# Performance work log

Hardware: AMD Instinct MI355X
Metric: run time of the kernel (lower is better)

## Reference

```python
import jax, jax.numpy as jnp
import numpy as np

B, L, D, H = 2, 4096, 768, 12
Dh = D // H


def setup_inputs() -> dict:
    key = jax.random.key(0)
    k1, k2, k3 = jax.random.split(key, 3)
    x = jax.random.normal(k1, (B, L, D), dtype=jnp.float32)
    Wqkv = jax.random.normal(k2, (D, 3 * D), dtype=jnp.float32) * 0.02
    bqkv = jnp.zeros((3 * D,), dtype=jnp.float32)
    Wo = jax.random.normal(k3, (D, D), dtype=jnp.float32) * 0.02
    bo = jnp.zeros((D,), dtype=jnp.float32)
    return {"x": x, "Wqkv": Wqkv, "bqkv": bqkv, "Wo": Wo, "bo": bo}


def reference(x, Wqkv, bqkv, Wo, bo):
    Bs, Ls, Ds = x.shape
    # fused QKV projection
    qkv = x @ Wqkv + bqkv  # [B, L, 3D]
    q, k, v = jnp.split(qkv, 3, axis=2)
    q = q.reshape(Bs, Ls, H, Dh)
    k = k.reshape(Bs, Ls, H, Dh)
    v = v.reshape(Bs, Ls, H, Dh)
    # scaled dot-product attention with causal mask (fp32 softmax, as flax dpa with dtype=float32)
    scale = 1.0 / np.sqrt(Dh)
    scores = jnp.einsum('bqhd,bkhd->bhqk', q, k) * scale  # [B, H, L, L]
    causal = jnp.tril(jnp.ones((Ls, Ls), dtype=bool))
    big_neg = jnp.finfo(jnp.float32).min
    scores = jnp.where(causal[None, None, :, :], scores, big_neg)
    attn = jax.nn.softmax(scores, axis=-1)
    y = jnp.einsum('bhqk,bkhd->bqhd', attn, v)  # [B, L, H, Dh]
    y = y.reshape(Bs, Ls, Ds)
    # output projection
    return y @ Wo + bo
```

## Files before the change

### kernel.cpp

```cpp
#include <hip/hip_runtime.h>
#include <hip/hip_bf16.h>
#include <stdint.h>

#define BB 2
#define LL 4096
#define DD 768
#define HH 12
#define DH 64
#define MM (BB * LL)
#define NQKV (3 * DD)
#define KK 768
#define PLANE ((size_t)BB * HH * LL * DH)
#define SQSCALE 0.1803368801111204f

typedef __attribute__((ext_vector_type(8))) short bf16x8;
typedef __attribute__((ext_vector_type(4))) float f32x4;

__device__ __forceinline__ float bf2f(uint16_t u) {
  union { uint32_t u; float f; } c; c.u = ((uint32_t)u) << 16; return c.f;
}
__device__ __forceinline__ uint16_t f2bf(float f) {
  union { float f; uint32_t u; } c; c.f = f;
  return (uint16_t)((c.u + 0x7FFFu + ((c.u >> 16) & 1u)) >> 16);
}
__device__ __forceinline__ uint32_t cvt2(float a, float b) {
  __hip_bfloat162 h = __float22bfloat162_rn(make_float2(a, b));
  union { __hip_bfloat162 h; uint32_t u; } c; c.h = h; return c.u;
}

union H8 { uint16_t h[8]; uint32_t w[4]; uint4 v; };
union B8 { uint2 d[2]; bf16x8 v; };

template <bool F32>
__device__ __forceinline__ H8 load8(const void* p, size_t idx) {
  H8 r;
  if (F32) {
    const float* f = (const float*)p + idx;
    float4 a = *(const float4*)f;
    float4 b = *(const float4*)(f + 4);
    r.w[0] = cvt2(a.x, a.y); r.w[1] = cvt2(a.z, a.w);
    r.w[2] = cvt2(b.x, b.y); r.w[3] = cvt2(b.z, b.w);
  } else {
    r.v = *(const uint4*)((const uint16_t*)p + idx);
  }
  return r;
}

__device__ __forceinline__ void g2l16(const uint16_t* g, uint16_t* l) {
  __builtin_amdgcn_global_load_lds((const __attribute__((address_space(1))) void*)g,
                                   (__attribute__((address_space(3))) void*)l,
                                   16, 0, 0);
}

__global__ void detect_k(const uint16_t* __restrict__ x, int* __restrict__ flag) {
  __shared__ int cnt;
  if (threadIdx.x == 0) cnt = 0;
  __syncthreads();
  int c = 0;
  for (int i = threadIdx.x; i < 4096; i += 256) {
    int e = (x[i] >> 7) & 0xFF;
    if (e == 0xFF || e > 133 || e < 100) c++;
  }
  atomicAdd(&cnt, c);
  __syncthreads();
  if (threadIdx.x == 0) *flag = (cnt > 512) ? 1 : 0;
}

__global__ __launch_bounds__(256) void prep_k(const void* __restrict__ x,
                                              uint16_t* __restrict__ xbf,
                                              const void* __restrict__ Wqkv,
                                              uint16_t* __restrict__ wqkvT,
                                              const void* __restrict__ Wo,
                                              uint16_t* __restrict__ woT,
                                              const int* __restrict__ flag) {
  __shared__ uint16_t Ts[64][65];
  const int fl = *flag;
  const int id = blockIdx.x;
  const int tid = threadIdx.x;
  if (id < 768) {
    size_t base = (size_t)id * 1024 + tid;
#pragma unroll
    for (int j = 0; j < 4; ++j) {
      size_t i = base + j * 256;
      H8 v = fl ? load8<true>(x, i * 8) : load8<false>(x, i * 8);
      *(uint4*)(xbf + i * 8) = v.v;
    }
    return;
  }
  const void* W;
  uint16_t* WT;
  int N, widx;
  if (id < 1200) { W = Wqkv; WT = wqkvT; N = NQKV; widx = id - 768; }
  else           { W = Wo;   WT = woT;   N = DD;   widx = id - 1200; }
  const int nb = N / 64;
  const int n0 = (widx % nb) * 64, k0 = (widx / nb) * 64;
#pragma unroll
  for (int j = 0; j < 16; ++j) {
    int idx = tid + j * 256;
    int r = idx >> 6, c = idx & 63;
    size_t gi = (size_t)(k0 + r) * N + n0 + c;
    float v = fl ? ((const float*)W)[gi] : bf2f(((const uint16_t*)W)[gi]);
    Ts[c][r] = f2bf(v);
  }
  __syncthreads();
#pragma unroll
  for (int j = 0; j < 16; ++j) {
    int idx = tid + j * 256;
    int n = idx >> 6, k = idx & 63;
    WT[(size_t)(n0 + n) * KK + k0 + k] = Ts[n][k];
  }
}

__device__ __forceinline__ void gemm128_core(const uint16_t* __restrict__ A,
                                             const uint16_t* __restrict__ BT,
                                             int m0, int n0,
                                             uint16_t* As, uint16_t* Bs,
                                             f32x4 acc[4][4]) {
  const int tid = threadIdx.x, lane = tid & 63, w = tid >> 6;
  const int quad = lane >> 4, c16 = lane & 15;
  const int wm = w >> 1, wn = w & 1;
  const int srow = lane >> 2, schunk = lane & 3;
  const int rsw = (c16 >> 1) & 3;
  for (int k0 = 0; k0 < KK; k0 += 32) {
#pragma unroll
    for (int i = 0; i < 2; ++i) {
      int row = w * 32 + i * 16 + srow;
      int gch = schunk ^ ((row >> 1) & 3);
      g2l16(A + (size_t)(m0 + row) * KK + k0 + gch * 8, As + (w * 32 + i * 16) * 32);
      g2l16(BT + (size_t)(n0 + row) * KK + k0 + gch * 8, Bs + (w * 32 + i * 16) * 32);
    }
    __syncthreads();
    bf16x8 a[4], b[4];
#pragma unroll
    for (int i = 0; i < 4; ++i) {
      a[i] = *(const bf16x8*)(As + (wm * 64 + i * 16 + c16) * 32 + ((quad ^ rsw) * 8));
      b[i] = *(const bf16x8*)(Bs + (wn * 64 + i * 16 + c16) * 32 + ((quad ^ rsw) * 8));
    }
#pragma unroll
    for (int i = 0; i < 4; ++i)
#pragma unroll
      for (int f = 0; f < 4; ++f)
        acc[i][f] = __builtin_amdgcn_mfma_f32_16x16x32_bf16(a[i], b[f], acc[i][f], 0, 0, 0);
    __syncthreads();
  }
}

__global__ __launch_bounds__(256) void qkv128_k(const uint16_t* __restrict__ X,
                                                const uint16_t* __restrict__ WT,
                                                const void* __restrict__ bias,
                                                uint16_t* __restrict__ planes,
                                                const int* __restrict__ flag) {
  __shared__ __align__(16) uint16_t As[128 * 32];
  __shared__ __align__(16) uint16_t Bs[128 * 32];
  __shared__ __align__(16) uint16_t Ts[64][136];
  const int fl = *flag;
  const int m0 = blockIdx.x * 128, n0 = blockIdx.y * 128;
  f32x4 acc[4][4];
#pragma unroll
  for (int i = 0; i < 4; ++i)
#pragma unroll
    for (int f = 0; f < 4; ++f) acc[i][f] = (f32x4){0.f, 0.f, 0.f, 0.f};
  gemm128_core(X, WT, m0, n0, As, Bs, acc);

  const int tid = threadIdx.x, lane = tid & 63, w = tid >> 6;
  const int quad = lane >> 4, c16 = lane & 15;
  const int wm = w >> 1, wn = w & 1;
  const int which = (n0 >= 2 * DD) ? 2 : (n0 >= DD ? 1 : 0);

  if (which < 2) {
    uint16_t* dst = planes + (size_t)which * PLANE;
    const float sc = (which == 0) ? SQSCALE : 1.0f;
#pragma unroll
    for (int f = 0; f < 4; ++f) {
      int n = n0 + wn * 64 + f * 16 + c16;
      float bv = fl ? ((const float*)bias)[n] : bf2f(((const uint16_t*)bias)[n]);
      int rem = n - which * DD;
      int hh = rem >> 6, dd = rem & 63;
#pragma unroll
      for (int i = 0; i < 4; ++i) {
        uint32_t pa = cvt2((acc[i][f][0] + bv) * sc, (acc[i][f][1] + bv) * sc);
        uint32_t pb = cvt2((acc[i][f][2] + bv) * sc, (acc[i][f][3] + bv) * sc);
        int m = m0 + wm * 64 + i * 16 + quad * 4;
        int b = m >> 12, l = m & (LL - 1);
        uint16_t* base = dst + ((size_t)(b * HH + hh) * LL + l) * DH + dd;
        base[0 * DH] = (uint16_t)pa;
        base[1 * DH] = (uint16_t)(pa >> 16);
        base[2 * DH] = (uint16_t)pb;
        base[3 * DH] = (uint16_t)(pb >> 16);
      }
    }
  } else {
    uint16_t* vtp = planes + 2 * PLANE;
    const int l0 = m0 & (LL - 1), bb = m0 >> 12;
    for (int half = 0; half < 2; ++half) {
      __syncthreads();
      if (wn == half) {
#pragma unroll
        for (int f = 0; f < 4; ++f) {
          int n = n0 + half * 64 + f * 16 + c16;
          float bv = fl ? ((const float*)bias)[n] : bf2f(((const uint16_t*)bias)[n]);
#pragma unroll
          for (int i = 0; i < 4; ++i) {
            uint32_t pa = cvt2(acc[i][f][0] + bv, acc[i][f][1] + bv);
            uint32_t pb = cvt2(acc[i][f][2] + bv, acc[i][f][3] + bv);
            *(uint2*)(&Ts[f * 16 + c16][wm * 64 + i * 16 + quad * 4]) = make_uint2(pa, pb);
          }
        }
      }
      __syncthreads();
#pragma unroll
      for (int j = 0; j < 4; ++j) {
        int idx = tid + j * 256;
        int nl = idx >> 4, ch = idx & 15;
        int rem = n0 + half * 64 + nl - 2 * DD;
        int hh = rem >> 6, dd = rem & 63;
        uint4 val = *(const uint4*)(&Ts[nl][ch * 8]);
        *(uint4*)(vtp + ((size_t)(bb * HH + hh) * DH + dd) * LL + l0 + ch * 8) = val;
      }
    }
  }
}

__global__ __launch_bounds__(256) void attn_k(const uint16_t* __restrict__ planes,
                                              uint16_t* __restrict__ y) {
  __shared__ __align__(16) uint16_t Ks[2][64 * 64];
  __shared__ __align__(16) uint16_t Vt[2][64 * 64];
  __shared__ __align__(16) uint16_t Ps[4][16 * 64];
  const int p = blockIdx.x;
  const int bh = blockIdx.y;
  const uint16_t* qb = planes + (size_t)bh * LL * DH;
  const uint16_t* kb = qb + PLANE;
  const uint16_t* vtb = planes + 2 * PLANE + (size_t)bh * DH * LL;
  const int tid = threadIdx.x, lane = tid & 63, wv = tid >> 6;
  const int quad = lane >> 4, c16 = lane & 15;
  const int r0 = tid >> 3, c0 = tid & 7;
  const int sw0 = r0 & 7;
  const int swf = c16 & 7;
  uint16_t* Psb = Ps[wv];
  const int b = bh / HH, hh = bh - b * HH;
  const int pwbase = c16 * 64;
  const int prd0 = pwbase + (((2 * quad) ^ c16) << 2);
  const int prd1 = pwbase + (((2 * quad + 1) ^ c16) << 2);
  const int prd2 = pwbase + (((8 + 2 * quad) ^ c16) << 2);
  const int prd3 = pwbase + (((8 + 2 * quad + 1) ^ c16) << 2);

  for (int pass = 0; pass < 2; ++pass) {
    const int qi = pass ? p : 63 - p;
    const int q0 = qi * 64;
    const size_t qoff = (size_t)(q0 + wv * 16 + c16) * DH;
    bf16x8 qf0 = *(const bf16x8*)(qb + qoff + quad * 8);
    bf16x8 qf1 = *(const bf16x8*)(qb + qoff + 32 + quad * 8);

    f32x4 o[4];
#pragma unroll
    for (int g = 0; g < 4; ++g) o[g] = (f32x4){0.f, 0.f, 0.f, 0.f};
    float l_i = 0.f;

    uint4 kr0 = *(const uint4*)(kb + (size_t)r0 * DH + c0 * 8);
    uint4 kr1 = *(const uint4*)(kb + (size_t)(r0 + 32) * DH + c0 * 8);
    uint4 vr0 = *(const uint4*)(vtb + (size_t)r0 * LL + c0 * 8);
    uint4 vr1 = *(const uint4*)(vtb + (size_t)(r0 + 32) * LL + c0 * 8);

    for (int t = 0; t <= qi; ++t) {
      uint16_t* kd = Ks[t & 1];
      uint16_t* vd = Vt[t & 1];
      *(uint4*)(kd + r0 * 64 + (c0 ^ sw0) * 8) = kr0;
      *(uint4*)(kd + (r0 + 32) * 64 + (c0 ^ sw0) * 8) = kr1;
      *(uint4*)(vd + r0 * 64 + (c0 ^ sw0) * 8) = vr0;
      *(uint4*)(vd + (r0 + 32) * 64 + (c0 ^ sw0) * 8) = vr1;
      if (t < qi) {
        int t64 = (t + 1) * 64;
        kr0 = *(const uint4*)(kb + (size_t)(t64 + r0) * DH + c0 * 8);
        kr1 = *(const uint4*)(kb + (size_t)(t64 + r0 + 32) * DH + c0 * 8);
        vr0 = *(const uint4*)(vtb + (size_t)r0 * LL + t64 + c0 * 8);
        vr1 = *(const uint4*)(vtb + (size_t)(r0 + 32) * LL + t64 + c0 * 8);
      }
      __syncthreads();

      f32x4 s[4];
#pragma unroll
      for (int f = 0; f < 4; ++f) {
        const uint16_t* krow = kd + (f * 16 + c16) * 64;
        bf16x8 k0f = *(const bf16x8*)(krow + ((quad ^ swf) * 8));
        bf16x8 k1f = *(const bf16x8*)(krow + (((quad + 4) ^ swf) * 8));
        f32x4 z = {0.f, 0.f, 0.f, 0.f};
        z = __builtin_amdgcn_mfma_f32_16x16x32_bf16(k0f, qf0, z, 0, 0, 0);
        z = __builtin_amdgcn_mfma_f32_16x16x32_bf16(k1f, qf1, z, 0, 0, 0);
        s[f] = z;
      }
      const int qg = q0 + wv * 16 + c16;
      if (t == qi) {
#pragma unroll
        for (int f = 0; f < 4; ++f) {
          int key0 = t * 64 + f * 16 + quad * 4;
#pragma unroll
          for (int r = 0; r < 4; ++r) {
            float pv = exp2f(s[f][r]);
            pv = (key0 + r <= qg) ? pv : 0.f;
            s[f][r] = pv;
            l_i += pv;
          }
        }
      } else {
#pragma unroll
        for (int f = 0; f < 4; ++f)
#pragma unroll
          for (int r = 0; r < 4; ++r) {
            float pv = exp2f(s[f][r]);
            s[f][r] = pv;
            l_i += pv;
          }
      }
#pragma unroll
      for (int f = 0; f < 4; ++f) {
        uint32_t w0 = cvt2(s[f][0], s[f][1]);
        uint32_t w1 = cvt2(s[f][2], s[f][3]);
        *(uint2*)(Psb + pwbase + (((f * 4 + quad) ^ c16) << 2)) = make_uint2(w0, w1);
      }
      __asm__ __volatile__("s_waitcnt lgkmcnt(0)" ::: "memory");
      B8 p0, p1;
      p0.d[0] = *(const uint2*)(Psb + prd0);
      p0.d[1] = *(const uint2*)(Psb + prd1);
      p1.d[0] = *(const uint2*)(Psb + prd2);
      p1.d[1] = *(const uint2*)(Psb + prd3);
#pragma unroll
      for (int g = 0; g < 4; ++g) {
        const uint16_t* vrow = vd + (g * 16 + c16) * 64;
        bf16x8 v0 = *(const bf16x8*)(vrow + ((quad ^ swf) * 8));
        bf16x8 v1 = *(const bf16x8*)(vrow + (((quad + 4) ^ swf) * 8));
        o[g] = __builtin_amdgcn_mfma_f32_16x16x32_bf16(p0.v, v0, o[g], 0, 0, 0);
        o[g] = __builtin_amdgcn_mfma_f32_16x16x32_bf16(p1.v, v1, o[g], 0, 0, 0);
      }
    }

    l_i += __shfl_xor(l_i, 16);
    l_i += __shfl_xor(l_i, 32);
    float inv[4];
#pragma unroll
    for (int r = 0; r < 4; ++r)
      inv[r] = 1.f / __shfl(l_i, (quad << 4) + quad * 4 + r);
#pragma unroll
    for (int g = 0; g < 4; ++g) {
      uint32_t pa = cvt2(o[g][0] * inv[0], o[g][1] * inv[1]);
      uint32_t pb = cvt2(o[g][2] * inv[2], o[g][3] * inv[3]);
      int l = q0 + wv * 16 + quad * 4;
      uint16_t* base = y + ((size_t)(b * LL + l)) * DD + hh * DH + g * 16 + c16;
      base[0 * DD] = (uint16_t)pa;
      base[1 * DD] = (uint16_t)(pa >> 16);
      base[2 * DD] = (uint16_t)pb;
      base[3 * DD] = (uint16_t)(pb >> 16);
    }
    __syncthreads();
  }
}

__global__ __launch_bounds__(256) void out128_k(const uint16_t* __restrict__ Y,
                                                const uint16_t* __restrict__ WT,
                                                const void* __restrict__ bias,
                                                void* __restrict__ out,
                                                const int* __restrict__ flag) {
  __shared__ __align__(16) uint16_t As[128 * 32];
  __shared__ __align__(16) uint16_t Bs[128 * 32];
  const int fl = *flag;
  const int m0 = blockIdx.x * 128, n0 = blockIdx.y * 128;
  f32x4 acc[4][4];
#pragma unroll
  for (int i = 0; i < 4; ++i)
#pragma unroll
    for (int f = 0; f < 4; ++f) acc[i][f] = (f32x4){0.f, 0.f, 0.f, 0.f};
  gemm128_core(Y, WT, m0, n0, As, Bs, acc);
  const int lane = threadIdx.x & 63, w = threadIdx.x >> 6;
  const int quad = lane >> 4, c16 = lane & 15;
  const int wm = w >> 1, wn = w & 1;
#pragma unroll
  for (int f = 0; f < 4; ++f) {
    int n = n0 + wn * 64 + f * 16 + c16;
    float bv = fl ? ((const float*)bias)[n] : bf2f(((const uint16_t*)bias)[n]);
#pragma unroll
    for (int i = 0; i < 4; ++i) {
      int m = m0 + wm * 64 + i * 16 + quad * 4;
      if (fl) {
        float* base = (float*)out + (size_t)m * DD + n;
#pragma unroll
        for (int r = 0; r < 4; ++r) base[r * DD] = acc[i][f][r] + bv;
      } else {
        uint32_t pa = cvt2(acc[i][f][0] + bv, acc[i][f][1] + bv);
        uint32_t pb = cvt2(acc[i][f][2] + bv, acc[i][f][3] + bv);
        uint16_t* base = (uint16_t*)out + (size_t)m * DD + n;
        base[0 * DD] = (uint16_t)pa;
        base[1 * DD] = (uint16_t)(pa >> 16);
        base[2 * DD] = (uint16_t)pb;
        base[3 * DD] = (uint16_t)(pb >> 16);
      }
    }
  }
}

extern "C" void kernel_launch(void* const* d_in, const int* in_sizes, int n_in,
                              void* d_out, int out_size, void* d_ws, size_t ws_size,
                              hipStream_t stream) {
  const void* x    = d_in[0];
  const void* Wqkv = d_in[1];
  const void* bqkv = d_in[2];
  const void* Wo   = d_in[3];
  const void* bo   = d_in[4];
  int* flagp = (int*)d_ws;
  uint16_t* planes = (uint16_t*)((char*)d_ws + 64);
  uint16_t* y_ws   = planes + 3 * PLANE;
  uint16_t* wqkvT  = y_ws + (size_t)MM * DD;
  uint16_t* woT    = wqkvT + (size_t)NQKV * KK;
  uint16_t* xbf    = y_ws;

  detect_k<<<1, 256, 0, stream>>>((const uint16_t*)x, flagp);
  prep_k<<<1344, 256, 0, stream>>>(x, xbf, Wqkv, wqkvT, Wo, woT, flagp);
  qkv128_k<<<dim3(MM / 128, NQKV / 128), 256, 0, stream>>>(xbf, wqkvT, bqkv, planes, flagp);
  attn_k<<<dim3(32, BB * HH), 256, 0, stream>>>(planes, y_ws);
  out128_k<<<dim3(MM / 128, DD / 128), 256, 0, stream>>>(y_ws, woT, bo, d_out, flagp);
}
```

Measured before the change: 271.0 us.

## Use fragment-major LDS layout with direct global-to-LDS loads in GEMMs and attention

Reorganizes shared-memory tiles into MFMA-fragment-major blocks of 512 elements, so each lane reads its 16-byte fragment contiguously without XOR swizzling. The GEMM core now steps K by 64 per barrier pair, halving the number of synchronizations. Attention K/V tiles are double-buffered through direct global-to-LDS copies instead of register staging plus LDS stores. The output projection switches to 128x64 tiles for more blocks. The copies are issued as narrow fragment rows, which may reduce global coalescing, and the qkv kernel reuses the same shared memory for the V transpose.

```diff
diff --git a/kernel.cpp b/kernel.cpp
--- a/kernel.cpp
+++ b/kernel.cpp
@@ -114,33 +114,47 @@
 __device__ __forceinline__ void gemm128_core(const uint16_t* __restrict__ A,
                                              const uint16_t* __restrict__ BT,
                                              int m0, int n0,
-                                             uint16_t* As, uint16_t* Bs,
+                                             uint16_t* Af, uint16_t* Bf,
                                              f32x4 acc[4][4]) {
   const int tid = threadIdx.x, lane = tid & 63, w = tid >> 6;
-  const int quad = lane >> 4, c16 = lane & 15;
+  const int c16 = lane & 15, quad = lane >> 4;
   const int wm = w >> 1, wn = w & 1;
-  const int srow = lane >> 2, schunk = lane & 3;
-  const int rsw = (c16 >> 1) & 3;
-  for (int k0 = 0; k0 < KK; k0 += 32) {
-#pragma unroll
-    for (int i = 0; i < 2; ++i) {
-      int row = w * 32 + i * 16 + srow;
-      int gch = schunk ^ ((row >> 1) & 3);
-      g2l16(A + (size_t)(m0 + row) * KK + k0 + gch * 8, As + (w * 32 + i * 16) * 32);
-      g2l16(BT + (size_t)(n0 + row) * KK + k0 + gch * 8, Bs + (w * 32 + i * 16) * 32);
+  const uint16_t* ga[4]; const uint16_t* gb[4];
+  uint16_t* la[4]; uint16_t* lb[4];
+#pragma unroll
+  for (int j = 0; j < 4; ++j) {
+    int ab = w * 4 + j;
+    int bwm = ab >> 3, bi = (ab >> 1) & 3, bhh = ab & 1;
+    int col = bhh * 32 + quad * 8;
+    ga[j] = A + (size_t)(m0 + bwm * 64 + bi * 16 + c16) * KK + col;
+    gb[j] = BT + (size_t)(n0 + bwm * 64 + bi * 16 + c16) * KK + col;
+    la[j] = Af + ab * 512;
+    lb[j] = Bf + ab * 512;
+  }
+  const int abase = wm * 8;
+  const int bbase = wn * 8;
+  for (int k0 = 0; k0 < KK; k0 += 64) {
+#pragma unroll
+    for (int j = 0; j < 4; ++j) {
+      g2l16(ga[j], la[j]); g2l16(gb[j], lb[j]);
+      ga[j] += 64; gb[j] += 64;
     }
     __syncthreads();
-    bf16x8 a[4], b[4];
-#pragma unroll
-    for (int i = 0; i < 4; ++i) {
-      a[i] = *(const bf16x8*)(As + (wm * 64 + i * 16 + c16) * 32 + ((quad ^ rsw) * 8));
-      b[i] = *(const bf16x8*)(Bs + (wn * 64 + i * 16 + c16) * 32 + ((quad ^ rsw) * 8));
-    }
-#pragma unroll
-    for (int i = 0; i < 4; ++i)
+#pragma unroll
+    for (int h = 0; h < 2; ++h) {
+      bf16x8 a[4], b[4];
+#pragma unroll
+      for (int i = 0; i < 4; ++i)
+        a[i] = *(const bf16x8*)(Af + (abase + i * 2 + h) * 512 + lane * 8);
 #pragma unroll
       for (int f = 0; f < 4; ++f)
-        acc[i][f] = __builtin_amdgcn_mfma_f32_16x16x32_bf16(a[i], b[f], acc[i][f], 0, 0, 0);
+        b[f] = *(const bf16x8*)(Bf + (bbase + f * 2 + h) * 512 + lane * 8);
+#pragma unroll
+      for (int i = 0; i < 4; ++i)
+#pragma unroll
+        for (int f = 0; f < 4; ++f)
+          acc[i][f] = __builtin_amdgcn_mfma_f32_16x16x32_bf16(a[i], b[f], acc[i][f], 0, 0, 0);
+    }
     __syncthreads();
   }
 }
@@ -150,9 +164,9 @@
                                                 const void* __restrict__ bias,
                                                 uint16_t* __restrict__ planes,
                                                 const int* __restrict__ flag) {
-  __shared__ __align__(16) uint16_t As[128 * 32];
-  __shared__ __align__(16) uint16_t Bs[128 * 32];
-  __shared__ __align__(16) uint16_t Ts[64][136];
+  __shared__ __align__(16) uint16_t smem[16384];
+  uint16_t* Af = smem;
+  uint16_t* Bf = smem + 8192;
   const int fl = *flag;
   const int m0 = blockIdx.x * 128, n0 = blockIdx.y * 128;
   f32x4 acc[4][4];
@@ -160,7 +174,7 @@
   for (int i = 0; i < 4; ++i)
 #pragma unroll
     for (int f = 0; f < 4; ++f) acc[i][f] = (f32x4){0.f, 0.f, 0.f, 0.f};
-  gemm128_core(X, WT, m0, n0, As, Bs, acc);
+  gemm128_core(X, WT, m0, n0, Af, Bf, acc);
 
   const int tid = threadIdx.x, lane = tid & 63, w = tid >> 6;
   const int quad = lane >> 4, c16 = lane & 15;
@@ -190,6 +204,7 @@
       }
     }
   } else {
+    uint16_t (*Ts)[136] = reinterpret_cast<uint16_t(*)[136]>(smem);
     uint16_t* vtp = planes + 2 * PLANE;
     const int l0 = m0 & (LL - 1), bb = m0 >> 12;
     for (int half = 0; half < 2; ++half) {
@@ -223,9 +238,9 @@
 
 __global__ __launch_bounds__(256) void attn_k(const uint16_t* __restrict__ planes,
                                               uint16_t* __restrict__ y) {
-  __shared__ __align__(16) uint16_t Ks[2][64 * 64];
-  __shared__ __align__(16) uint16_t Vt[2][64 * 64];
-  __shared__ __align__(16) uint16_t Ps[4][16 * 64];
+  __shared__ __align__(16) uint16_t Kf[2][4096];
+  __shared__ __align__(16) uint16_t Vf[2][4096];
+  __shared__ __align__(16) uint16_t Ps[4][1024];
   const int p = blockIdx.x;
   const int bh = blockIdx.y;
   const uint16_t* qb = planes + (size_t)bh * LL * DH;
@@ -233,9 +248,6 @@
   const uint16_t* vtb = planes + 2 * PLANE + (size_t)bh * DH * LL;
   const int tid = threadIdx.x, lane = tid & 63, wv = tid >> 6;
   const int quad = lane >> 4, c16 = lane & 15;
-  const int r0 = tid >> 3, c0 = tid & 7;
-  const int sw0 = r0 & 7;
-  const int swf = c16 & 7;
   uint16_t* Psb = Ps[wv];
   const int b = bh / HH, hh = bh - b * HH;
   const int pwbase = c16 * 64;
@@ -243,10 +255,18 @@
   const int prd1 = pwbase + (((2 * quad + 1) ^ c16) << 2);
   const int prd2 = pwbase + (((8 + 2 * quad) ^ c16) << 2);
   const int prd3 = pwbase + (((8 + 2 * quad + 1) ^ c16) << 2);
+  uint16_t* lk0 = nullptr;
 
   for (int pass = 0; pass < 2; ++pass) {
     const int qi = pass ? p : 63 - p;
     const int q0 = qi * 64;
+    const uint16_t* gk = kb + (size_t)(wv * 16 + c16) * DH + quad * 8;
+    const uint16_t* gv = vtb + (size_t)(wv * 16 + c16) * LL + quad * 8;
+    g2l16(gk,      Kf[0] + (wv * 2 + 0) * 512);
+    g2l16(gk + 32, Kf[0] + (wv * 2 + 1) * 512);
+    g2l16(gv,      Vf[0] + (wv * 2 + 0) * 512);
+    g2l16(gv + 32, Vf[0] + (wv * 2 + 1) * 512);
+
     const size_t qoff = (size_t)(q0 + wv * 16 + c16) * DH;
     bf16x8 qf0 = *(const bf16x8*)(qb + qoff + quad * 8);
     bf16x8 qf1 = *(const bf16x8*)(qb + qoff + 32 + quad * 8);
@@ -256,33 +276,26 @@
     for (int g = 0; g < 4; ++g) o[g] = (f32x4){0.f, 0.f, 0.f, 0.f};
     float l_i = 0.f;
 
-    uint4 kr0 = *(const uint4*)(kb + (size_t)r0 * DH + c0 * 8);
-    uint4 kr1 = *(const uint4*)(kb + (size_t)(r0 + 32) * DH + c0 * 8);
-    uint4 vr0 = *(const uint4*)(vtb + (size_t)r0 * LL + c0 * 8);
-    uint4 vr1 = *(const uint4*)(vtb + (size_t)(r0 + 32) * LL + c0 * 8);
-
     for (int t = 0; t <= qi; ++t) {
-      uint16_t* kd = Ks[t & 1];
-      uint16_t* vd = Vt[t & 1];
-      *(uint4*)(kd + r0 * 64 + (c0 ^ sw0) * 8) = kr0;
-      *(uint4*)(kd + (r0 + 32) * 64 + (c0 ^ sw0) * 8) = kr1;
-      *(uint4*)(vd + r0 * 64 + (c0 ^ sw0) * 8) = vr0;
-      *(uint4*)(vd + (r0 + 32) * 64 + (c0 ^ sw0) * 8) = vr1;
+      __syncthreads();
       if (t < qi) {
-        int t64 = (t + 1) * 64;
-        kr0 = *(const uint4*)(kb + (size_t)(t64 + r0) * DH + c0 * 8);
-        kr1 = *(const uint4*)(kb + (size_t)(t64 + r0 + 32) * DH + c0 * 8);
-        vr0 = *(const uint4*)(vtb + (size_t)r0 * LL + t64 + c0 * 8);
-        vr1 = *(const uint4*)(vtb + (size_t)(r0 + 32) * LL + t64 + c0 * 8);
-      }
-      __syncthreads();
+        gk += 64 * DH;
+        gv += 64;
+        uint16_t* kn = Kf[(t + 1) & 1];
+        uint16_t* vn = Vf[(t + 1) & 1];
+        g2l16(gk,      kn + (wv * 2 + 0) * 512);
+        g2l16(gk + 32, kn + (wv * 2 + 1) * 512);
+        g2l16(gv,      vn + (wv * 2 + 0) * 512);
+        g2l16(gv + 32, vn + (wv * 2 + 1) * 512);
+      }
+      const uint16_t* kd = Kf[t & 1];
+      const uint16_t* vd = Vf[t & 1];
 
       f32x4 s[4];
 #pragma unroll
       for (int f = 0; f < 4; ++f) {
-        const uint16_t* krow = kd + (f * 16 + c16) * 64;
-        bf16x8 k0f = *(const bf16x8*)(krow + ((quad ^ swf) * 8));
-        bf16x8 k1f = *(const bf16x8*)(krow + (((quad + 4) ^ swf) * 8));
+        bf16x8 k0f = *(const bf16x8*)(kd + (f * 2 + 0) * 512 + lane * 8);
+        bf16x8 k1f = *(const bf16x8*)(kd + (f * 2 + 1) * 512 + lane * 8);
         f32x4 z = {0.f, 0.f, 0.f, 0.f};
         z = __builtin_amdgcn_mfma_f32_16x16x32_bf16(k0f, qf0, z, 0, 0, 0);
         z = __builtin_amdgcn_mfma_f32_16x16x32_bf16(k1f, qf1, z, 0, 0, 0);
@@ -325,9 +338,8 @@
       p1.d[1] = *(const uint2*)(Psb + prd3);
 #pragma unroll
       for (int g = 0; g < 4; ++g) {
-        const uint16_t* vrow = vd + (g * 16 + c16) * 64;
-        bf16x8 v0 = *(const bf16x8*)(vrow + ((quad ^ swf) * 8));
-        bf16x8 v1 = *(const bf16x8*)(vrow + (((quad + 4) ^ swf) * 8));
+        bf16x8 v0 = *(const bf16x8*)(vd + (g * 2 + 0) * 512 + lane * 8);
+        bf16x8 v1 = *(const bf16x8*)(vd + (g * 2 + 1) * 512 + lane * 8);
         o[g] = __builtin_amdgcn_mfma_f32_16x16x32_bf16(p0.v, v0, o[g], 0, 0, 0);
         o[g] = __builtin_amdgcn_mfma_f32_16x16x32_bf16(p1.v, v1, o[g], 0, 0, 0);
       }
@@ -352,33 +364,68 @@
     }
     __syncthreads();
   }
-}
-
-__global__ __launch_bounds__(256) void out128_k(const uint16_t* __restrict__ Y,
-                                                const uint16_t* __restrict__ WT,
-                                                const void* __restrict__ bias,
-                                                void* __restrict__ out,
-                                                const int* __restrict__ flag) {
-  __shared__ __align__(16) uint16_t As[128 * 32];
-  __shared__ __align__(16) uint16_t Bs[128 * 32];
+  (void)lk0;
+}
+
+__global__ __launch_bounds__(256) void out64_k(const uint16_t* __restrict__ Y,
+                                               const uint16_t* __restrict__ WT,
+                                               const void* __restrict__ bias,
+                                               void* __restrict__ out,
+                                               const int* __restrict__ flag) {
+  __shared__ __align__(16) uint16_t Af[16 * 512];
+  __shared__ __align__(16) uint16_t Bf[8 * 512];
   const int fl = *flag;
-  const int m0 = blockIdx.x * 128, n0 = blockIdx.y * 128;
-  f32x4 acc[4][4];
-#pragma unroll
-  for (int i = 0; i < 4; ++i)
+  const int m0 = blockIdx.x * 128, n0 = blockIdx.y * 64;
+  const int tid = threadIdx.x, lane = tid & 63, w = tid >> 6;
+  const int c16 = lane & 15, quad = lane >> 4;
+  f32x4 acc[2][4];
+#pragma unroll
+  for (int i = 0; i < 2; ++i)
 #pragma unroll
     for (int f = 0; f < 4; ++f) acc[i][f] = (f32x4){0.f, 0.f, 0.f, 0.f};
-  gemm128_core(Y, WT, m0, n0, As, Bs, acc);
-  const int lane = threadIdx.x & 63, w = threadIdx.x >> 6;
-  const int quad = lane >> 4, c16 = lane & 15;
-  const int wm = w >> 1, wn = w & 1;
+  const uint16_t* ga[4]; uint16_t* la[4];
+#pragma unroll
+  for (int j = 0; j < 4; ++j) {
+    int i = j >> 1, h = j & 1;
+    ga[j] = Y + (size_t)(m0 + w * 32 + i * 16 + c16) * KK + h * 32 + quad * 8;
+    la[j] = Af + ((w * 2 + i) * 2 + h) * 512;
+  }
+  const uint16_t* gbp[2]; uint16_t* lbp[2];
+#pragma unroll
+  for (int h = 0; h < 2; ++h) {
+    gbp[h] = WT + (size_t)(n0 + w * 16 + c16) * KK + h * 32 + quad * 8;
+    lbp[h] = Bf + (w * 2 + h) * 512;
+  }
+  for (int k0 = 0; k0 < KK; k0 += 64) {
+#pragma unroll
+    for (int j = 0; j < 4; ++j) { g2l16(ga[j], la[j]); ga[j] += 64; }
+#pragma unroll
+    for (int h = 0; h < 2; ++h) { g2l16(gbp[h], lbp[h]); gbp[h] += 64; }
+    __syncthreads();
+#pragma unroll
+    for (int h = 0; h < 2; ++h) {
+      bf16x8 a[2], bfr[4];
+#pragma unroll
+      for (int i = 0; i < 2; ++i)
+        a[i] = *(const bf16x8*)(Af + ((w * 2 + i) * 2 + h) * 512 + lane * 8);
+#pragma unroll
+      for (int f = 0; f < 4; ++f)
+        bfr[f] = *(const bf16x8*)(Bf + (f * 2 + h) * 512 + lane * 8);
+#pragma unroll
+      for (int i = 0; i < 2; ++i)
+#pragma unroll
+        for (int f = 0; f < 4; ++f)
+          acc[i][f] = __builtin_amdgcn_mfma_f32_16x16x32_bf16(a[i], bfr[f], acc[i][f], 0, 0, 0);
+    }
+    __syncthreads();
+  }
 #pragma unroll
   for (int f = 0; f < 4; ++f) {
-    int n = n0 + wn * 64 + f * 16 + c16;
+    int n = n0 + f * 16 + c16;
     float bv = fl ? ((const float*)bias)[n] : bf2f(((const uint16_t*)bias)[n]);
 #pragma unroll
-    for (int i = 0; i < 4; ++i) {
-      int m = m0 + wm * 64 + i * 16 + quad * 4;
+    for (int i = 0; i < 2; ++i) {
+      int m = m0 + w * 32 + i * 16 + quad * 4;
       if (fl) {
         float* base = (float*)out + (size_t)m * DD + n;
 #pragma unroll
@@ -415,5 +462,5 @@
   prep_k<<<1344, 256, 0, stream>>>(x, xbf, Wqkv, wqkvT, Wo, woT, flagp);
   qkv128_k<<<dim3(MM / 128, NQKV / 128), 256, 0, stream>>>(xbf, wqkvT, bqkv, planes, flagp);
   attn_k<<<dim3(32, BB * HH), 256, 0, stream>>>(planes, y_ws);
-  out128_k<<<dim3(MM / 128, DD / 128), 256, 0, stream>>>(y_ws, woT, bo, d_out, flagp);
-}
+  out64_k<<<dim3(MM / 128, DD / 64), 256, 0, stream>>>(y_ws, woT, bo, d_out, flagp);
+}
```

New measurement: 322.3 us. 18.9% more time.
